# Optimization experiments

Measured on AMD Instinct MI355X. Metric: run time of the kernel, lower is better.

## Reference

```python
import jax, jax.numpy as jnp
import numpy as np

H = 16  # num_heads
EPS_DEN = 1e-6


def setup_inputs() -> dict:
    key = jax.random.key(0)
    k1, k2, k3 = jax.random.split(key, 3)
    x = jax.random.normal(k1, (2, 4096, 2048), dtype=jnp.float32)
    # torch Linear weights stored as [in, out] so y = x @ W
    w_qkv = jax.random.normal(k2, (2048, 6144), dtype=jnp.float32) * 0.02
    w_out = jax.random.normal(k3, (2048, 2048), dtype=jnp.float32) * 0.02
    decay_param = jnp.full((H,), 0.95, dtype=jnp.float32)
    return {"x": x, "w_qkv": w_qkv, "w_out": w_out, "decay_param": decay_param}


def _decay_scan(x, decay, init):
    """Inclusive causal scan: s_t = decay * s_{t-1} + x_t, s_{-1} = init.
    x: [B,H,T,D], decay: [1,H,1], init: [B,H,D] -> [B,H,T,D].
    (Numerically stable recurrence form; identical math to the torch
    decay-weighted cumsum closed form.)"""
    xT = jnp.moveaxis(x, 2, 0)  # [T,B,H,D]

    def step(s, xt):
        s = decay * s + xt  # decay [1,H,1] broadcasts over [B,H,D]
        return s, s

    _, ys = jax.lax.scan(step, init, xT)
    return jnp.moveaxis(ys, 0, 2)  # [B,H,T,D]


def _phi(z):
    return jax.nn.elu(z) + 1.0


def reference(x, w_qkv, w_out, decay_param):
    B, T, Hid = x.shape
    D = Hid // H
    qkv = x @ w_qkv  # [B,T,3*Hid]
    q, k, v = jnp.split(qkv, 3, axis=-1)

    def to_bhtd(t):
        return t.reshape(B, T, H, D).transpose(0, 2, 1, 3)

    q = _phi(to_bhtd(q))
    k = _phi(to_bhtd(k))
    v = to_bhtd(v)

    decay = jax.nn.sigmoid(decay_param).reshape(1, H, 1)  # per-head decay in (0,1)
    init = jnp.zeros((B, H, D), dtype=x.dtype)

    running_kv = _decay_scan(k * v, decay, init)  # [B,H,T,D]
    running_ksum = _decay_scan(k, decay, init)    # [B,H,T,D]

    den = jnp.clip(jnp.sum(q * running_ksum, axis=-1, keepdims=True), EPS_DEN, None)
    out = q * running_kv / den  # [B,H,T,D]
    out = out.transpose(0, 2, 1, 3).reshape(B, T, Hid) @ w_out

    new_kv = running_kv[:, :, -1, :]
    new_ksum = running_ksum[:, :, -1, :]
    return out, new_kv, new_ksum
```

## Files before the change

kernel.cpp:

```cpp
#include <hip/hip_runtime.h>
#include <hip/hip_bf16.h>
#include <stdint.h>

constexpr int NB = 2;
constexpr int NT = 4096;
constexpr int NH = 16;
constexpr int ND = 128;
constexpr int HID = NH * ND;
constexpr int QKV_N = 3 * HID;
constexpr int ROWS = NB * NT;
constexpr int CHUNK = 64;
constexpr int NCH = NT / CHUNK;

typedef __bf16 bf16x8 __attribute__((ext_vector_type(8)));
typedef float  f32x4  __attribute__((ext_vector_type(4)));

__device__ inline unsigned short f2bf(float f) {
    unsigned u = __builtin_bit_cast(unsigned, f);
    u += 0x7fffu + ((u >> 16) & 1u);
    return (unsigned short)(u >> 16);
}
__device__ inline float bf2f(unsigned short b) {
    unsigned u = ((unsigned)b) << 16;
    return __builtin_bit_cast(float, u);
}

__global__ void cast_kernel(const float* __restrict__ in,
                            unsigned short* __restrict__ out, size_t n4) {
    size_t i = blockIdx.x * (size_t)blockDim.x + threadIdx.x;
    size_t stride = (size_t)gridDim.x * blockDim.x;
    for (; i < n4; i += stride) {
        float4 v = reinterpret_cast<const float4*>(in)[i];
        ushort4 o;
        o.x = f2bf(v.x); o.y = f2bf(v.y); o.z = f2bf(v.z); o.w = f2bf(v.w);
        reinterpret_cast<ushort4*>(out)[i] = o;
    }
}

__global__ __launch_bounds__(256) void transpose_cast(
        const float* __restrict__ in, unsigned short* __restrict__ out,
        int R, int Cn) {
    __shared__ float tile[32][33];
    const int c  = threadIdx.x & 31;
    const int r8 = threadIdx.x >> 5;
    const int r0 = blockIdx.y * 32, c0 = blockIdx.x * 32;
    #pragma unroll
    for (int i = 0; i < 32; i += 8)
        tile[r8 + i][c] = in[(size_t)(r0 + r8 + i) * Cn + c0 + c];
    __syncthreads();
    #pragma unroll
    for (int i = 0; i < 32; i += 8)
        out[(size_t)(c0 + r8 + i) * R + r0 + c] = f2bf(tile[c][r8 + i]);
}


#define WAITV(N) asm volatile("s_waitcnt vmcnt(" #N ")" ::: "memory")
#define LGKM0()  asm volatile("s_waitcnt lgkmcnt(0)" ::: "memory")
#define BAR()    do { asm volatile("" ::: "memory"); \
                      __builtin_amdgcn_s_barrier();  \
                      asm volatile("" ::: "memory"); } while (0)

__device__ __forceinline__ void gll(const unsigned short* src, unsigned short* dst) {
    __builtin_amdgcn_global_load_lds(
        (const __attribute__((address_space(1))) void*)src,
        (__attribute__((address_space(3))) void*)dst, 16, 0, 0);
}

__device__ __forceinline__ void stage_a(const unsigned short* Ag, int K, int k0,
                                        unsigned short* lds, int sub,
                                        int wid, int lane) {
    const int rl = wid * 8 + (lane >> 3);
    const int ce = ((lane & 7) ^ (lane >> 3)) * 8;
    #pragma unroll
    for (int j = 0; j < 2; ++j) {
        int row = j * 128 + sub * 64;
        gll(Ag + (size_t)(row + rl) * K + k0 + ce,
            lds + (row + wid * 8) * 64);
    }
}
__device__ __forceinline__ void stage_b(const unsigned short* Bg, int K, int k0,
                                        unsigned short* lds, int sub,
                                        int wid, int lane) {
    const int ce = ((lane & 7) ^ (lane >> 3)) * 8;
    const int rb = (wid >> 2) * 64 + sub * 32 + (wid & 3) * 8;
    #pragma unroll
    for (int j = 0; j < 2; ++j) {
        int rowbase = j * 128 + rb;
        gll(Bg + (size_t)(rowbase + (lane >> 3)) * K + k0 + ce,
            lds + rowbase * 64);
    }
}

__device__ __forceinline__ bf16x8 ld_frag(const unsigned short* tile,
                                          int r, int kk, int fq) {
    int slot = (kk * 4 + fq) ^ (r & 7);
    return *reinterpret_cast<const bf16x8*>(tile + r * 64 + slot * 8);
}

template <int MH>
__device__ __forceinline__ void read_a(const unsigned short* T, int wm,
                                       int fr, int fq, bf16x8 af[4][2]) {
    #pragma unroll
    for (int m = 0; m < 4; ++m) {
        int r = wm * 128 + MH * 64 + m * 16 + fr;
        af[m][0] = ld_frag(T, r, 0, fq);
        af[m][1] = ld_frag(T, r, 1, fq);
    }
}
template <int NHH>
__device__ __forceinline__ void read_b(const unsigned short* T, int wn,
                                       int fr, int fq, bf16x8 bfr[4][2]) {
    #pragma unroll
    for (int n = 0; n < 2; ++n) {
        int r = wn * 64 + NHH * 32 + n * 16 + fr;
        bfr[NHH * 2 + n][0] = ld_frag(T, r, 0, fq);
        bfr[NHH * 2 + n][1] = ld_frag(T, r, 1, fq);
    }
}

template <int MH, int NHH>
__device__ __forceinline__ void mfma_quad(f32x4 acc[8][4],
                                          const bf16x8 af[4][2],
                                          const bf16x8 bfr[4][2]) {
    __builtin_amdgcn_s_setprio(1);
    #pragma unroll
    for (int kk = 0; kk < 2; ++kk)
        #pragma unroll
        for (int m = 0; m < 4; ++m)
            #pragma unroll
            for (int n = 0; n < 2; ++n)
                acc[MH * 4 + m][NHH * 2 + n] =
                    __builtin_amdgcn_mfma_f32_16x16x32_bf16(
                        af[m][kk], bfr[NHH * 2 + n][kk],
                        acc[MH * 4 + m][NHH * 2 + n], 0, 0, 0);
    __builtin_amdgcn_s_setprio(0);
}

template <typename OUT_T>
__global__ __launch_bounds__(512, 2) void gemm256(
        const unsigned short* __restrict__ A,
        const unsigned short* __restrict__ Bt,
        OUT_T* __restrict__ C,
        int M, int N, int K, int nbx, int cpx) {
    __shared__ unsigned short As[2][256 * 64];
    __shared__ unsigned short Bs[2][256 * 64];

    const int bid = blockIdx.x;
    const int wk  = (bid & 7) * cpx + (bid >> 3);
    const int bx  = wk % nbx, by = wk / nbx;
    const int tid = threadIdx.x, wid = tid >> 6, lane = tid & 63;
    const int wm  = wid >> 2, wn = wid & 3;
    const int fr  = lane & 15, fq = lane >> 4;

    const unsigned short* Ag = A  + (size_t)by * 256 * K;
    const unsigned short* Bg = Bt + (size_t)bx * 256 * K;

    f32x4 acc[8][4] = {};
    bf16x8 aflo[4][2], afhi[4][2], bfr[4][2];

    stage_b(Bg, K, 0, Bs[0], 0, wid, lane);
    stage_b(Bg, K, 0, Bs[0], 1, wid, lane);
    stage_a(Ag, K, 0, As[0], 1, wid, lane);
    stage_a(Ag, K, 0, As[0], 0, wid, lane);
    stage_b(Bg, K, 64, Bs[1], 0, wid, lane);
    stage_b(Bg, K, 64, Bs[1], 1, wid, lane);
    stage_a(Ag, K, 64, As[1], 1, wid, lane);
    stage_a(Ag, K, 64, As[1], 0, wid, lane);
    WAITV(8);
    BAR();
    read_a<0>(As[0], wm, fr, fq, aflo);

    const int NK = K / 64;
    for (int k = 0; k < NK / 2 - 1; ++k) {
        const int kA = (2 * k + 2) * 64;
        const int kB = (2 * k + 3) * 64;
        read_b<0>(Bs[0], wn, fr, fq, bfr);
        BAR(); LGKM0();
        mfma_quad<0, 0>(acc, aflo, bfr);
        BAR();
        read_b<1>(Bs[0], wn, fr, fq, bfr);
        stage_b(Bg, K, kA, Bs[0], 0, wid, lane);
        BAR(); LGKM0();
        mfma_quad<0, 1>(acc, aflo, bfr);
        BAR();
        read_a<1>(As[0], wm, fr, fq, afhi);
        stage_b(Bg, K, kA, Bs[0], 1, wid, lane);
        BAR(); LGKM0();
        mfma_quad<1, 1>(acc, afhi, bfr);
        BAR();
        WAITV(4);
        stage_a(Ag, K, kA, As[0], 1, wid, lane);
        stage_a(Ag, K, kA, As[0], 0, wid, lane);
        BAR();
        read_a<0>(As[1], wm, fr, fq, aflo);
        mfma_quad<1, 0>(acc, afhi, bfr);
        BAR();
        read_b<0>(Bs[1], wn, fr, fq, bfr);
        BAR(); LGKM0();
        mfma_quad<0, 0>(acc, aflo, bfr);
        BAR();
        read_b<1>(Bs[1], wn, fr, fq, bfr);
        stage_b(Bg, K, kB, Bs[1], 0, wid, lane);
        BAR(); LGKM0();
        mfma_quad<0, 1>(acc, aflo, bfr);
        BAR();
        read_a<1>(As[1], wm, fr, fq, afhi);
        stage_b(Bg, K, kB, Bs[1], 1, wid, lane);
        BAR(); LGKM0();
        mfma_quad<1, 1>(acc, afhi, bfr);
        BAR();
        WAITV(4);
        stage_a(Ag, K, kB, As[1], 1, wid, lane);
        stage_a(Ag, K, kB, As[1], 0, wid, lane);
        BAR();
        read_a<0>(As[0], wm, fr, fq, aflo);
        mfma_quad<1, 0>(acc, afhi, bfr);
        BAR();
    }
    read_b<0>(Bs[0], wn, fr, fq, bfr);
    BAR(); LGKM0(); mfma_quad<0, 0>(acc, aflo, bfr); BAR();
    read_b<1>(Bs[0], wn, fr, fq, bfr);
    BAR(); LGKM0(); mfma_quad<0, 1>(acc, aflo, bfr); BAR();
    read_a<1>(As[0], wm, fr, fq, afhi);
    BAR(); LGKM0(); mfma_quad<1, 1>(acc, afhi, bfr); BAR();
    WAITV(0); BAR();
    read_a<0>(As[1], wm, fr, fq, aflo);
    mfma_quad<1, 0>(acc, afhi, bfr); BAR();
    read_b<0>(Bs[1], wn, fr, fq, bfr);
    BAR(); LGKM0(); mfma_quad<0, 0>(acc, aflo, bfr); BAR();
    read_b<1>(Bs[1], wn, fr, fq, bfr);
    BAR(); LGKM0(); mfma_quad<0, 1>(acc, aflo, bfr); BAR();
    read_a<1>(As[1], wm, fr, fq, afhi);
    BAR(); LGKM0(); mfma_quad<1, 1>(acc, afhi, bfr); BAR();
    mfma_quad<1, 0>(acc, afhi, bfr);

    const int bm = by * 256, bn = bx * 256;
    #pragma unroll
    for (int m = 0; m < 8; ++m) {
        #pragma unroll
        for (int n = 0; n < 4; ++n) {
            #pragma unroll
            for (int r = 0; r < 4; ++r) {
                int row = bm + wm * 128 + m * 16 + fq * 4 + r;
                int col = bn + wn * 64 + n * 16 + fr;
                float v = acc[m][n][r];
                if constexpr (sizeof(OUT_T) == 2)
                    C[(size_t)row * N + col] = (OUT_T)f2bf(v);
                else
                    C[(size_t)row * N + col] = (OUT_T)v;
            }
        }
    }
}

__device__ inline float phi_f(float z) { return z > 0.f ? z + 1.f : __expf(z); }
__device__ inline float sigmoid_f(float z) { return 1.f / (1.f + __expf(-z)); }

__global__ void scan_pass1(const unsigned short* __restrict__ qkv,
                           const float* __restrict__ decay_param,
                           float* __restrict__ fkv, float* __restrict__ fk) {
    const int blk = blockIdx.x;
    const int c = blk % NCH;
    const int h = (blk / NCH) % NH;
    const int b = blk / (NCH * NH);
    const int lane = threadIdx.x;
    const float dec = sigmoid_f(decay_param[h]);

    float skv0 = 0.f, skv1 = 0.f, sk0 = 0.f, sk1 = 0.f;
    const unsigned short* base =
        qkv + ((size_t)b * NT + (size_t)c * CHUNK) * QKV_N + h * ND;
    for (int t = 0; t < CHUNK; ++t) {
        const unsigned short* r = base + (size_t)t * QKV_N;
        unsigned kp = *reinterpret_cast<const unsigned*>(r + HID + 2 * lane);
        unsigned vp = *reinterpret_cast<const unsigned*>(r + 2 * HID + 2 * lane);
        float k0 = phi_f(bf2f((unsigned short)(kp & 0xffff)));
        float k1 = phi_f(bf2f((unsigned short)(kp >> 16)));
        float v0 = bf2f((unsigned short)(vp & 0xffff));
        float v1 = bf2f((unsigned short)(vp >> 16));
        skv0 = fmaf(dec, skv0, k0 * v0);
        skv1 = fmaf(dec, skv1, k1 * v1);
        sk0  = fmaf(dec, sk0,  k0);
        sk1  = fmaf(dec, sk1,  k1);
    }
    size_t o = (size_t)blk * ND + 2 * lane;
    *reinterpret_cast<float2*>(&fkv[o]) = make_float2(skv0, skv1);
    *reinterpret_cast<float2*>(&fk[o])  = make_float2(sk0, sk1);
}

__global__ void scan_pass2(const float* __restrict__ fkv, const float* __restrict__ fk,
                           const float* __restrict__ decay_param,
                           float* __restrict__ ckv, float* __restrict__ ck,
                           float* __restrict__ out_states) {
    const int bh = blockIdx.x;
    const int h = bh % NH;
    const int lane = threadIdx.x;
    const float dec = sigmoid_f(decay_param[h]);
    const float dL = powf(dec, (float)CHUNK);

    float Skv0 = 0.f, Skv1 = 0.f, Sk0 = 0.f, Sk1 = 0.f;
    for (int c = 0; c < NCH; ++c) {
        size_t o = ((size_t)bh * NCH + c) * ND + 2 * lane;
        *reinterpret_cast<float2*>(&ckv[o]) = make_float2(Skv0, Skv1);
        *reinterpret_cast<float2*>(&ck[o])  = make_float2(Sk0, Sk1);
        float2 fv = *reinterpret_cast<const float2*>(&fkv[o]);
        float2 fs = *reinterpret_cast<const float2*>(&fk[o]);
        Skv0 = fmaf(dL, Skv0, fv.x);
        Skv1 = fmaf(dL, Skv1, fv.y);
        Sk0  = fmaf(dL, Sk0,  fs.x);
        Sk1  = fmaf(dL, Sk1,  fs.y);
    }
    size_t so = (size_t)bh * ND + 2 * lane;
    *reinterpret_cast<float2*>(&out_states[so]) = make_float2(Skv0, Skv1);
    *reinterpret_cast<float2*>(&out_states[NB * NH * ND + so]) = make_float2(Sk0, Sk1);
}

__global__ void scan_pass3(const unsigned short* __restrict__ qkv,
                           const float* __restrict__ decay_param,
                           const float* __restrict__ ckv, const float* __restrict__ ck,
                           unsigned short* __restrict__ attn) {
    const int blk = blockIdx.x;
    const int c = blk % NCH;
    const int h = (blk / NCH) % NH;
    const int b = blk / (NCH * NH);
    const int lane = threadIdx.x;
    const float dec = sigmoid_f(decay_param[h]);

    size_t co = (size_t)blk * ND + 2 * lane;
    float2 cv = *reinterpret_cast<const float2*>(&ckv[co]);
    float2 cs = *reinterpret_cast<const float2*>(&ck[co]);
    float skv0 = cv.x, skv1 = cv.y, sk0 = cs.x, sk1 = cs.y;

    const unsigned short* base =
        qkv + ((size_t)b * NT + (size_t)c * CHUNK) * QKV_N + h * ND;
    unsigned short* abase =
        attn + ((size_t)b * NT + (size_t)c * CHUNK) * HID + h * ND;

    for (int t = 0; t < CHUNK; ++t) {
        const unsigned short* r = base + (size_t)t * QKV_N;
        unsigned qp = *reinterpret_cast<const unsigned*>(r + 2 * lane);
        unsigned kp = *reinterpret_cast<const unsigned*>(r + HID + 2 * lane);
        unsigned vp = *reinterpret_cast<const unsigned*>(r + 2 * HID + 2 * lane);
        float q0 = phi_f(bf2f((unsigned short)(qp & 0xffff)));
        float q1 = phi_f(bf2f((unsigned short)(qp >> 16)));
        float k0 = phi_f(bf2f((unsigned short)(kp & 0xffff)));
        float k1 = phi_f(bf2f((unsigned short)(kp >> 16)));
        float v0 = bf2f((unsigned short)(vp & 0xffff));
        float v1 = bf2f((unsigned short)(vp >> 16));
        skv0 = fmaf(dec, skv0, k0 * v0);
        skv1 = fmaf(dec, skv1, k1 * v1);
        sk0  = fmaf(dec, sk0,  k0);
        sk1  = fmaf(dec, sk1,  k1);
        float den = fmaf(q0, sk0, q1 * sk1);
        #pragma unroll
        for (int m = 1; m < 64; m <<= 1) den += __shfl_xor(den, m, 64);
        den = fmaxf(den, 1e-6f);
        float inv = 1.f / den;
        unsigned o = ((unsigned)f2bf(q1 * skv1 * inv) << 16) |
                     (unsigned)f2bf(q0 * skv0 * inv);
        *reinterpret_cast<unsigned*>(abase + (size_t)t * HID + 2 * lane) = o;
    }
}

extern "C" void kernel_launch(void* const* d_in, const int* in_sizes, int n_in,
                              void* d_out, int out_size, void* d_ws, size_t ws_size,
                              hipStream_t stream) {
    const float* x      = (const float*)d_in[0];
    const float* w_qkv  = (const float*)d_in[1];
    const float* w_out  = (const float*)d_in[2];
    const float* decayp = (const float*)d_in[3];
    float* out = (float*)d_out;

    char* ws = (char*)d_ws;
    unsigned short* xb     = (unsigned short*)ws;
    unsigned short* wqkvT  = xb    + (size_t)ROWS * HID;
    unsigned short* woutT  = wqkvT + (size_t)QKV_N * HID;
    unsigned short* qkvb   = woutT + (size_t)HID * HID;
    unsigned short* attnb  = qkvb  + (size_t)ROWS * QKV_N;
    float* fkv = (float*)(attnb + (size_t)ROWS * HID);
    float* fk  = fkv + (size_t)NB * NH * NCH * ND;
    float* ckv = fk  + (size_t)NB * NH * NCH * ND;
    float* ck  = ckv + (size_t)NB * NH * NCH * ND;

    cast_kernel<<<2048, 256, 0, stream>>>(x, xb, (size_t)ROWS * HID / 4);
    dim3 tg1(QKV_N / 32, HID / 32);
    transpose_cast<<<tg1, 256, 0, stream>>>(w_qkv, wqkvT, HID, QKV_N);
    dim3 tg2(HID / 32, HID / 32);
    transpose_cast<<<tg2, 256, 0, stream>>>(w_out, woutT, HID, HID);

    {
        int nbx = QKV_N / 256, nwg = (ROWS / 256) * nbx;
        gemm256<unsigned short><<<nwg, 512, 0, stream>>>(
            xb, wqkvT, qkvb, ROWS, QKV_N, HID, nbx, nwg / 8);
    }

    scan_pass1<<<NB * NH * NCH, 64, 0, stream>>>(qkvb, decayp, fkv, fk);
    scan_pass2<<<NB * NH, 64, 0, stream>>>(fkv, fk, decayp, ckv, ck,
                                           out + (size_t)ROWS * HID);
    scan_pass3<<<NB * NH * NCH, 64, 0, stream>>>(qkvb, decayp, ckv, ck, attnb);

    {
        int nbx = HID / 256, nwg = (ROWS / 256) * nbx;
        gemm256<float><<<nwg, 512, 0, stream>>>(
            attnb, woutT, out, ROWS, HID, HID, nbx, nwg / 8);
    }
}
```

Before: 388.3 us.

## Stage GEMM epilogue through LDS for vectorized stores; drop explicit lgkmcnt waits

Removes the explicit s_waitcnt lgkmcnt(0) after each barrier in the GEMM main loop and replaces the barrier macro with a raw s_barrier asm. The epilogue now writes each wave's accumulator tile into LDS slabs reused from the A/B buffers. It then reads rows back and issues 16-byte vectorized global stores instead of scattered scalar stores. Dropping the lgkm waits relies on the compiler inserting the waits needed before the MFMAs consume the LDS-read fragments. The raw asm barrier may hide LDS dependencies from the compiler and risks races or stale fragments.

```diff
diff --git a/kernel.cpp b/kernel.cpp
--- a/kernel.cpp
+++ b/kernel.cpp
@@ -55,10 +55,7 @@
 
 
 #define WAITV(N) asm volatile("s_waitcnt vmcnt(" #N ")" ::: "memory")
-#define LGKM0()  asm volatile("s_waitcnt lgkmcnt(0)" ::: "memory")
-#define BAR()    do { asm volatile("" ::: "memory"); \
-                      __builtin_amdgcn_s_barrier();  \
-                      asm volatile("" ::: "memory"); } while (0)
+#define BAR()    asm volatile("s_barrier" ::: "memory")
 
 __device__ __forceinline__ void gll(const unsigned short* src, unsigned short* dst) {
     __builtin_amdgcn_global_load_lds(
@@ -175,17 +172,17 @@
         const int kA = (2 * k + 2) * 64;
         const int kB = (2 * k + 3) * 64;
         read_b<0>(Bs[0], wn, fr, fq, bfr);
-        BAR(); LGKM0();
+        BAR();
         mfma_quad<0, 0>(acc, aflo, bfr);
         BAR();
         read_b<1>(Bs[0], wn, fr, fq, bfr);
         stage_b(Bg, K, kA, Bs[0], 0, wid, lane);
-        BAR(); LGKM0();
+        BAR();
         mfma_quad<0, 1>(acc, aflo, bfr);
         BAR();
         read_a<1>(As[0], wm, fr, fq, afhi);
         stage_b(Bg, K, kA, Bs[0], 1, wid, lane);
-        BAR(); LGKM0();
+        BAR();
         mfma_quad<1, 1>(acc, afhi, bfr);
         BAR();
         WAITV(4);
@@ -196,17 +193,17 @@
         mfma_quad<1, 0>(acc, afhi, bfr);
         BAR();
         read_b<0>(Bs[1], wn, fr, fq, bfr);
-        BAR(); LGKM0();
+        BAR();
         mfma_quad<0, 0>(acc, aflo, bfr);
         BAR();
         read_b<1>(Bs[1], wn, fr, fq, bfr);
         stage_b(Bg, K, kB, Bs[1], 0, wid, lane);
-        BAR(); LGKM0();
+        BAR();
         mfma_quad<0, 1>(acc, aflo, bfr);
         BAR();
         read_a<1>(As[1], wm, fr, fq, afhi);
         stage_b(Bg, K, kB, Bs[1], 1, wid, lane);
-        BAR(); LGKM0();
+        BAR();
         mfma_quad<1, 1>(acc, afhi, bfr);
         BAR();
         WAITV(4);
@@ -218,36 +215,64 @@
         BAR();
     }
     read_b<0>(Bs[0], wn, fr, fq, bfr);
-    BAR(); LGKM0(); mfma_quad<0, 0>(acc, aflo, bfr); BAR();
+    BAR(); mfma_quad<0, 0>(acc, aflo, bfr); BAR();
     read_b<1>(Bs[0], wn, fr, fq, bfr);
-    BAR(); LGKM0(); mfma_quad<0, 1>(acc, aflo, bfr); BAR();
+    BAR(); mfma_quad<0, 1>(acc, aflo, bfr); BAR();
     read_a<1>(As[0], wm, fr, fq, afhi);
-    BAR(); LGKM0(); mfma_quad<1, 1>(acc, afhi, bfr); BAR();
+    BAR(); mfma_quad<1, 1>(acc, afhi, bfr); BAR();
     WAITV(0); BAR();
     read_a<0>(As[1], wm, fr, fq, aflo);
     mfma_quad<1, 0>(acc, afhi, bfr); BAR();
     read_b<0>(Bs[1], wn, fr, fq, bfr);
-    BAR(); LGKM0(); mfma_quad<0, 0>(acc, aflo, bfr); BAR();
+    BAR(); mfma_quad<0, 0>(acc, aflo, bfr); BAR();
     read_b<1>(Bs[1], wn, fr, fq, bfr);
-    BAR(); LGKM0(); mfma_quad<0, 1>(acc, aflo, bfr); BAR();
+    BAR(); mfma_quad<0, 1>(acc, aflo, bfr); BAR();
     read_a<1>(As[1], wm, fr, fq, afhi);
-    BAR(); LGKM0(); mfma_quad<1, 1>(acc, afhi, bfr); BAR();
+    BAR(); mfma_quad<1, 1>(acc, afhi, bfr); BAR();
     mfma_quad<1, 0>(acc, afhi, bfr);
 
+    BAR();
+    unsigned short* slab = (wid < 4) ? (&As[0][0] + wid * 8192)
+                                     : (&Bs[0][0] + (wid - 4) * 8192);
     const int bm = by * 256, bn = bx * 256;
-    #pragma unroll
-    for (int m = 0; m < 8; ++m) {
+    if constexpr (sizeof(OUT_T) == 2) {
         #pragma unroll
-        for (int n = 0; n < 4; ++n) {
+        for (int m = 0; m < 8; ++m)
             #pragma unroll
-            for (int r = 0; r < 4; ++r) {
-                int row = bm + wm * 128 + m * 16 + fq * 4 + r;
-                int col = bn + wn * 64 + n * 16 + fr;
-                float v = acc[m][n][r];
-                if constexpr (sizeof(OUT_T) == 2)
-                    C[(size_t)row * N + col] = (OUT_T)f2bf(v);
-                else
-                    C[(size_t)row * N + col] = (OUT_T)v;
+            for (int n = 0; n < 4; ++n)
+                #pragma unroll
+                for (int r = 0; r < 4; ++r)
+                    slab[(m * 16 + fq * 4 + r) * 64 + n * 16 + fr] =
+                        f2bf(acc[m][n][r]);
+        #pragma unroll
+        for (int p = 0; p < 16; ++p) {
+            int row = p * 8 + (lane >> 3);
+            int c8  = (lane & 7) * 8;
+            bf16x8 v = *reinterpret_cast<const bf16x8*>(&slab[row * 64 + c8]);
+            *reinterpret_cast<bf16x8*>(
+                &((unsigned short*)C)[(size_t)(bm + wm * 128 + row) * N
+                                      + bn + wn * 64 + c8]) = v;
+        }
+    } else {
+        float* fslab = (float*)slab;
+        #pragma unroll
+        for (int h = 0; h < 2; ++h) {
+            #pragma unroll
+            for (int m = 0; m < 4; ++m)
+                #pragma unroll
+                for (int n = 0; n < 4; ++n)
+                    #pragma unroll
+                    for (int r = 0; r < 4; ++r)
+                        fslab[(m * 16 + fq * 4 + r) * 64 + n * 16 + fr] =
+                            acc[h * 4 + m][n][r];
+            #pragma unroll
+            for (int p = 0; p < 16; ++p) {
+                int row = p * 4 + (lane >> 4);
+                int c4  = (lane & 15) * 4;
+                f32x4 v = *reinterpret_cast<const f32x4*>(&fslab[row * 64 + c4]);
+                *reinterpret_cast<f32x4*>(
+                    &((float*)C)[(size_t)(bm + wm * 128 + h * 64 + row) * N
+                                 + bn + wn * 64 + c4]) = v;
             }
         }
     }
```

New measurement: 420.2 us. 1.08x slower.

## Restructure GEMM main loop into four-phase schedule with fewer barriers and lgkm waits

Applied to the files above, without the earlier changes.

Rewrites the GEMM K-loop schedule so that each phase loads both A halves and one B half, then issues a full column of MFMAs (16 per k-step). Global-to-LDS staging is reordered and spread across the phases with new vmcnt wait counts. The explicit lgkmcnt(0) waits and compiler memory fences around barriers are dropped, leaving ordering to the compiler. The goal is fewer barriers and stalls per K step and better overlap of loads with MFMA, at the cost of more live fragment registers and riskier hand-tuned synchronization.

```diff
diff --git a/kernel.cpp b/kernel.cpp
--- a/kernel.cpp
+++ b/kernel.cpp
@@ -55,10 +55,7 @@
 
 
 #define WAITV(N) asm volatile("s_waitcnt vmcnt(" #N ")" ::: "memory")
-#define LGKM0()  asm volatile("s_waitcnt lgkmcnt(0)" ::: "memory")
-#define BAR()    do { asm volatile("" ::: "memory"); \
-                      __builtin_amdgcn_s_barrier();  \
-                      asm volatile("" ::: "memory"); } while (0)
+#define BARB()   __builtin_amdgcn_s_barrier()
 
 __device__ __forceinline__ void gll(const unsigned short* src, unsigned short* dst) {
     __builtin_amdgcn_global_load_lds(
@@ -118,21 +115,31 @@
     }
 }
 
-template <int MH, int NHH>
-__device__ __forceinline__ void mfma_quad(f32x4 acc[8][4],
-                                          const bf16x8 af[4][2],
-                                          const bf16x8 bfr[4][2]) {
+template <int NHH>
+__device__ __forceinline__ void mfma_col(f32x4 acc[8][4],
+                                         const bf16x8 aflo[4][2],
+                                         const bf16x8 afhi[4][2],
+                                         const bf16x8 bfr[4][2]) {
     __builtin_amdgcn_s_setprio(1);
     #pragma unroll
-    for (int kk = 0; kk < 2; ++kk)
+    for (int kk = 0; kk < 2; ++kk) {
         #pragma unroll
         for (int m = 0; m < 4; ++m)
             #pragma unroll
             for (int n = 0; n < 2; ++n)
-                acc[MH * 4 + m][NHH * 2 + n] =
+                acc[m][NHH * 2 + n] =
                     __builtin_amdgcn_mfma_f32_16x16x32_bf16(
-                        af[m][kk], bfr[NHH * 2 + n][kk],
-                        acc[MH * 4 + m][NHH * 2 + n], 0, 0, 0);
+                        aflo[m][kk], bfr[NHH * 2 + n][kk],
+                        acc[m][NHH * 2 + n], 0, 0, 0);
+        #pragma unroll
+        for (int m = 0; m < 4; ++m)
+            #pragma unroll
+            for (int n = 0; n < 2; ++n)
+                acc[4 + m][NHH * 2 + n] =
+                    __builtin_amdgcn_mfma_f32_16x16x32_bf16(
+                        afhi[m][kk], bfr[NHH * 2 + n][kk],
+                        acc[4 + m][NHH * 2 + n], 0, 0, 0);
+    }
     __builtin_amdgcn_s_setprio(0);
 }
 
@@ -158,81 +165,78 @@
     f32x4 acc[8][4] = {};
     bf16x8 aflo[4][2], afhi[4][2], bfr[4][2];
 
+    stage_a(Ag, K, 0, As[0], 0, wid, lane);
+    stage_a(Ag, K, 0, As[0], 1, wid, lane);
     stage_b(Bg, K, 0, Bs[0], 0, wid, lane);
     stage_b(Bg, K, 0, Bs[0], 1, wid, lane);
-    stage_a(Ag, K, 0, As[0], 1, wid, lane);
-    stage_a(Ag, K, 0, As[0], 0, wid, lane);
+    stage_a(Ag, K, 64, As[1], 0, wid, lane);
+    stage_a(Ag, K, 64, As[1], 1, wid, lane);
     stage_b(Bg, K, 64, Bs[1], 0, wid, lane);
-    stage_b(Bg, K, 64, Bs[1], 1, wid, lane);
-    stage_a(Ag, K, 64, As[1], 1, wid, lane);
-    stage_a(Ag, K, 64, As[1], 0, wid, lane);
-    WAITV(8);
-    BAR();
-    read_a<0>(As[0], wm, fr, fq, aflo);
 
     const int NK = K / 64;
-    for (int k = 0; k < NK / 2 - 1; ++k) {
-        const int kA = (2 * k + 2) * 64;
-        const int kB = (2 * k + 3) * 64;
+    const int NITER = NK / 2;
+    for (int k = 0; k < NITER - 1; ++k) {
+        const int kT1 = (2 * k + 1) * 64;
+        const int kA  = (2 * k + 2) * 64;
+        const int kB  = (2 * k + 3) * 64;
+        WAITV(6);
+        stage_b(Bg, K, kT1, Bs[1], 1, wid, lane);
+        read_a<0>(As[0], wm, fr, fq, aflo);
+        read_a<1>(As[0], wm, fr, fq, afhi);
         read_b<0>(Bs[0], wn, fr, fq, bfr);
-        BAR(); LGKM0();
-        mfma_quad<0, 0>(acc, aflo, bfr);
-        BAR();
+        BARB();
+        mfma_col<0>(acc, aflo, afhi, bfr);
+        BARB();
+        stage_a(Ag, K, kA, As[0], 0, wid, lane);
+        stage_a(Ag, K, kA, As[0], 1, wid, lane);
+        stage_b(Bg, K, kA, Bs[0], 0, wid, lane);
         read_b<1>(Bs[0], wn, fr, fq, bfr);
-        stage_b(Bg, K, kA, Bs[0], 0, wid, lane);
-        BAR(); LGKM0();
-        mfma_quad<0, 1>(acc, aflo, bfr);
-        BAR();
+        BARB();
+        mfma_col<1>(acc, aflo, afhi, bfr);
+        BARB();
+        WAITV(8);
+        stage_b(Bg, K, kA, Bs[0], 1, wid, lane);
+        read_a<0>(As[1], wm, fr, fq, aflo);
+        read_a<1>(As[1], wm, fr, fq, afhi);
+        read_b<0>(Bs[1], wn, fr, fq, bfr);
+        BARB();
+        mfma_col<0>(acc, aflo, afhi, bfr);
+        BARB();
+        WAITV(8);
+        stage_a(Ag, K, kB, As[1], 0, wid, lane);
+        stage_a(Ag, K, kB, As[1], 1, wid, lane);
+        stage_b(Bg, K, kB, Bs[1], 0, wid, lane);
+        read_b<1>(Bs[1], wn, fr, fq, bfr);
+        BARB();
+        mfma_col<1>(acc, aflo, afhi, bfr);
+        BARB();
+    }
+    {
+        const int kT1 = (NK - 1) * 64;
+        WAITV(6);
+        stage_b(Bg, K, kT1, Bs[1], 1, wid, lane);
+        read_a<0>(As[0], wm, fr, fq, aflo);
         read_a<1>(As[0], wm, fr, fq, afhi);
-        stage_b(Bg, K, kA, Bs[0], 1, wid, lane);
-        BAR(); LGKM0();
-        mfma_quad<1, 1>(acc, afhi, bfr);
-        BAR();
-        WAITV(4);
-        stage_a(Ag, K, kA, As[0], 1, wid, lane);
-        stage_a(Ag, K, kA, As[0], 0, wid, lane);
-        BAR();
+        read_b<0>(Bs[0], wn, fr, fq, bfr);
+        BARB();
+        mfma_col<0>(acc, aflo, afhi, bfr);
+        BARB();
+        read_b<1>(Bs[0], wn, fr, fq, bfr);
+        BARB();
+        mfma_col<1>(acc, aflo, afhi, bfr);
+        BARB();
+        WAITV(2);
         read_a<0>(As[1], wm, fr, fq, aflo);
-        mfma_quad<1, 0>(acc, afhi, bfr);
-        BAR();
+        read_a<1>(As[1], wm, fr, fq, afhi);
         read_b<0>(Bs[1], wn, fr, fq, bfr);
-        BAR(); LGKM0();
-        mfma_quad<0, 0>(acc, aflo, bfr);
-        BAR();
+        BARB();
+        mfma_col<0>(acc, aflo, afhi, bfr);
+        BARB();
+        WAITV(0);
         read_b<1>(Bs[1], wn, fr, fq, bfr);
-        stage_b(Bg, K, kB, Bs[1], 0, wid, lane);
-        BAR(); LGKM0();
-        mfma_quad<0, 1>(acc, aflo, bfr);
-        BAR();
-        read_a<1>(As[1], wm, fr, fq, afhi);
-        stage_b(Bg, K, kB, Bs[1], 1, wid, lane);
-        BAR(); LGKM0();
-        mfma_quad<1, 1>(acc, afhi, bfr);
-        BAR();
-        WAITV(4);
-        stage_a(Ag, K, kB, As[1], 1, wid, lane);
-        stage_a(Ag, K, kB, As[1], 0, wid, lane);
-        BAR();
-        read_a<0>(As[0], wm, fr, fq, aflo);
-        mfma_quad<1, 0>(acc, afhi, bfr);
-        BAR();
-    }
-    read_b<0>(Bs[0], wn, fr, fq, bfr);
-    BAR(); LGKM0(); mfma_quad<0, 0>(acc, aflo, bfr); BAR();
-    read_b<1>(Bs[0], wn, fr, fq, bfr);
-    BAR(); LGKM0(); mfma_quad<0, 1>(acc, aflo, bfr); BAR();
-    read_a<1>(As[0], wm, fr, fq, afhi);
-    BAR(); LGKM0(); mfma_quad<1, 1>(acc, afhi, bfr); BAR();
-    WAITV(0); BAR();
-    read_a<0>(As[1], wm, fr, fq, aflo);
-    mfma_quad<1, 0>(acc, afhi, bfr); BAR();
-    read_b<0>(Bs[1], wn, fr, fq, bfr);
-    BAR(); LGKM0(); mfma_quad<0, 0>(acc, aflo, bfr); BAR();
-    read_b<1>(Bs[1], wn, fr, fq, bfr);
-    BAR(); LGKM0(); mfma_quad<0, 1>(acc, aflo, bfr); BAR();
-    read_a<1>(As[1], wm, fr, fq, afhi);
-    BAR(); LGKM0(); mfma_quad<1, 1>(acc, afhi, bfr); BAR();
-    mfma_quad<1, 0>(acc, afhi, bfr);
+        BARB();
+        mfma_col<1>(acc, aflo, afhi, bfr);
+    }
 
     const int bm = by * 256, bn = bx * 256;
     #pragma unroll
```

Result: no change. 394.6 us (+1.6%).
